# Performance work log

Hardware: AMD Instinct MI355X
Metric: run time of the kernel (lower is better)

## Reference

```python
import jax, jax.numpy as jnp
import numpy as np

E = 5          # num_experts
TEMP = 1.0     # gate temperature


def setup_inputs() -> dict:
    key = jax.random.key(0)
    ks = jax.random.split(key, 12)
    B, C, H, W = 8, 256, 80, 80
    half, quarter = C // 2, C // 4  # 128, 64
    s = lambda fan_in: 1.0 / np.sqrt(fan_in)
    return {
        "x":    jax.random.normal(ks[0], (B, C, H, W), dtype=jnp.float32),
        # gate Linear(C -> E)
        "Wg":   jax.random.uniform(ks[1], (E, C), jnp.float32, -s(C), s(C)),
        "bg":   jax.random.uniform(ks[2], (E,), jnp.float32, -s(C), s(C)),
        # per-expert conv1x1 weights, stacked on expert axis
        "Wrgb": jax.random.uniform(ks[3], (E, half, half), jnp.float32, -s(half), s(half)),
        "brgb": jax.random.uniform(ks[4], (E, half), jnp.float32, -s(half), s(half)),
        "Wtir": jax.random.uniform(ks[5], (E, half, half), jnp.float32, -s(half), s(half)),
        "btir": jax.random.uniform(ks[6], (E, half), jnp.float32, -s(half), s(half)),
        # transform: conv1x1 half->quarter, ReLU, conv1x1 quarter->1
        "Wt1":  jax.random.uniform(ks[7], (E, quarter, half), jnp.float32, -s(half), s(half)),
        "bt1":  jax.random.uniform(ks[8], (E, quarter), jnp.float32, -s(half), s(half)),
        "Wt2":  jax.random.uniform(ks[9], (E, 1, quarter), jnp.float32, -s(quarter), s(quarter)),
        "bt2":  jax.random.uniform(ks[10], (E, 1), jnp.float32, -s(quarter), s(quarter)),
    }


def _gate(x, Wg, bg):
    # AdaptiveAvgPool2d(1) + Flatten + Linear; eval path (no training noise)
    pooled = x.mean(axis=(2, 3))                       # [B, C]
    logits = pooled @ Wg.T + bg                        # [B, E]
    # top-1 mask + masked softmax (argmax == topk(k=1), first index on ties)
    top1 = jnp.argmax(logits, axis=1)                  # [B]
    mask = jax.nn.one_hot(top1, E, dtype=bool)         # [B, E]
    masked = jnp.where(mask, logits, -jnp.inf)
    return jax.nn.softmax(masked / TEMP, axis=1)       # [B, E]


def _experts(x, Wrgb, brgb, Wtir, btir, Wt1, bt1, Wt2, bt2):
    half = x.shape[1] // 2
    xr, xt = x[:, :half], x[:, half:]                  # [B, half, H, W]
    # residual conv1x1 for all experts at once -> [B, E, half, H, W]
    Dr = xr[:, None] + jnp.einsum('bchw,eoc->beohw', xr, Wrgb) + brgb[None, :, :, None, None]
    Dt = xt[:, None] + jnp.einsum('bchw,eoc->beohw', xt, Wtir) + btir[None, :, :, None, None]

    def transform(D):
        h = jax.nn.relu(jnp.einsum('beohw,emo->bemhw', D, Wt1) + bt1[None, :, :, None, None])
        a = jnp.einsum('bemhw,ekm->bekhw', h, Wt2) + bt2[None, :, :, None, None]
        return jax.nn.sigmoid(a)                       # [B, E, 1, H, W]

    return transform(Dr) * Dr + transform(Dt) * Dt     # [B, E, half, H, W]


def reference(x, Wg, bg, Wrgb, brgb, Wtir, btir, Wt1, bt1, Wt2, bt2):
    weights = _gate(x, Wg, bg)                         # [B, E]
    Dfuse = _experts(x, Wrgb, brgb, Wtir, btir, Wt1, bt1, Wt2, bt2)
    # weighted sum over experts -> [B, half, H, W]
    return jnp.einsum('beohw,be->bohw', Dfuse, weights)
```

## Files before the change

kernel.cpp:

```cpp
#include <hip/hip_runtime.h>

#define HW    6400
#define CIN   256
#define HALF  128
#define QUART 64
#define NB    8
#define NE    5

typedef __attribute__((ext_vector_type(8))) short short8;
typedef __attribute__((ext_vector_type(4))) float f32x4;

__device__ __forceinline__ unsigned short f2bf(float f) {
    unsigned u = __builtin_bit_cast(unsigned, f);
    u = (u + 0x7FFFu + ((u >> 16) & 1u)) >> 16;
    return (unsigned short)u;
}

__global__ void pool_prep_kernel(const float* __restrict__ x,
                                 const float* __restrict__ Wrgb, const float* __restrict__ Wtir,
                                 const float* __restrict__ Wt1,
                                 float* __restrict__ pooled, unsigned short* __restrict__ bw) {
    int blk = blockIdx.x;
    if (blk < NB * CIN) {
        const float4* p = reinterpret_cast<const float4*>(x + (size_t)blk * HW);
        float s = 0.f;
        for (int i = threadIdx.x; i < HW / 4; i += 256) {
            float4 v = p[i];
            s += (v.x + v.y) + (v.z + v.w);
        }
        for (int off = 32; off > 0; off >>= 1) s += __shfl_down(s, off, 64);
        __shared__ float wsum[4];
        int wid = threadIdx.x >> 6, lane = threadIdx.x & 63;
        if (lane == 0) wsum[wid] = s;
        __syncthreads();
        if (threadIdx.x == 0)
            pooled[blk] = (wsum[0] + wsum[1] + wsum[2] + wsum[3]) * (1.0f / HW);
    } else {
        int i0 = (blk - NB * CIN) * 1024 + threadIdx.x;
#pragma unroll
        for (int j = 0; j < 4; ++j) {
            int i = i0 + j * 256;
            float v;
            if (i < 81920) {
                v = Wrgb[i];
                int m = i & 16383;
                if ((m >> 7) == (m & 127)) v += 1.0f;
            } else if (i < 163840) {
                int k = i - 81920;
                v = Wtir[k];
                int m = k & 16383;
                if ((m >> 7) == (m & 127)) v += 1.0f;
            } else {
                v = Wt1[i - 163840];
            }
            bw[i] = f2bf(v);
        }
    }
}

__launch_bounds__(256, 4)
__global__ void expert_kernel(const float* __restrict__ x,
                              const unsigned short* __restrict__ bW,
                              const float* __restrict__ brgb, const float* __restrict__ btir,
                              const float* __restrict__ bt1,
                              const float* __restrict__ Wt2, const float* __restrict__ bt2,
                              const float* __restrict__ pooled,
                              const float* __restrict__ Wg, const float* __restrict__ bg,
                              float* __restrict__ out) {
    __shared__ unsigned short lxr[8192];
    __shared__ unsigned short lxt[8192];
    __shared__ float psum[512];
    __shared__ float sfin[128];
    __shared__ int   se;

    const int b    = blockIdx.y;
    const int p0   = blockIdx.x * 64;
    const int t    = threadIdx.x;
    const int w    = __builtin_amdgcn_readfirstlane(t >> 6);
    const int lane = t & 63;
    const int lo   = lane & 15, hi = lane >> 4;

    {
        const int px = t & 63, cb = t >> 6;
        const float* xb = x + (size_t)b * CIN * HW + p0 + px;
        const int li = (px & 15) * 8;
        const int fb = (cb * 4 + (px >> 4)) * 512;
#pragma unroll
        for (int jg = 0; jg < 4; ++jg) {
            unsigned vr[4], vt[4];
#pragma unroll
            for (int jp = 0; jp < 4; ++jp) {
                int ch = cb * 32 + jg * 8 + jp * 2;
                float r0 = xb[(size_t)ch * HW];
                float r1 = xb[(size_t)(ch + 1) * HW];
                float t0 = xb[(size_t)(ch + HALF) * HW];
                float t1 = xb[(size_t)(ch + HALF + 1) * HW];
                vr[jp] = (unsigned)f2bf(r0) | ((unsigned)f2bf(r1) << 16);
                vt[jp] = (unsigned)f2bf(t0) | ((unsigned)f2bf(t1) << 16);
            }
            int si = fb + jg * 128 + li;
            *reinterpret_cast<uint4*>(&lxr[si]) = make_uint4(vr[0], vr[1], vr[2], vr[3]);
            *reinterpret_cast<uint4*>(&lxt[si]) = make_uint4(vt[0], vt[1], vt[2], vt[3]);
        }
    }

    if (t < 64) {
        float pv[4];
#pragma unroll
        for (int j = 0; j < 4; ++j) pv[j] = pooled[b * CIN + t * 4 + j];
        float best = -1e30f; int bi = 0;
        for (int e = 0; e < NE; ++e) {
            float part = 0.f;
#pragma unroll
            for (int j = 0; j < 4; ++j) part += pv[j] * Wg[e * CIN + t * 4 + j];
            for (int off = 32; off > 0; off >>= 1) part += __shfl_down(part, off, 64);
            part = __shfl(part, 0, 64);
            float logit = part + bg[e];
            if (logit > best) { best = logit; bi = e; }
        }
        if (t == 0) se = bi;
    }
    __syncthreads();

    const int e = __builtin_amdgcn_readfirstlane(se);
    const unsigned short* bWrgb = bW + (size_t)e * 16384;
    const unsigned short* bWtir = bW + 81920 + (size_t)e * 16384;
    const unsigned short* bWt1  = bW + 163840 + (size_t)e * 8192;

    f32x4 cr[2][4], ct[2][4];
    {
        f32x4 z = {0.f, 0.f, 0.f, 0.f};
#pragma unroll
        for (int i = 0; i < 2; ++i)
#pragma unroll
            for (int j = 0; j < 4; ++j) { cr[i][j] = z; ct[i][j] = z; }
    }
#pragma unroll
    for (int kt = 0; kt < 4; ++kt) {
        short8 bR[4], bT[4];
#pragma unroll
        for (int pt = 0; pt < 4; ++pt) {
            bR[pt] = *reinterpret_cast<const short8*>(&lxr[(kt * 4 + pt) * 512 + lane * 8]);
            bT[pt] = *reinterpret_cast<const short8*>(&lxt[(kt * 4 + pt) * 512 + lane * 8]);
        }
#pragma unroll
        for (int rt = 0; rt < 2; ++rt) {
            int row = w * 32 + rt * 16 + lo;
            short8 aR = *reinterpret_cast<const short8*>(&bWrgb[row * 128 + kt * 32 + hi * 8]);
            short8 aT = *reinterpret_cast<const short8*>(&bWtir[row * 128 + kt * 32 + hi * 8]);
#pragma unroll
            for (int pt = 0; pt < 4; ++pt) {
                cr[rt][pt] = __builtin_amdgcn_mfma_f32_16x16x32_bf16(aR, bR[pt], cr[rt][pt], 0, 0, 0);
                ct[rt][pt] = __builtin_amdgcn_mfma_f32_16x16x32_bf16(aT, bT[pt], ct[rt][pt], 0, 0, 0);
            }
        }
    }

    uint2 dbr[2][4], dbt[2][4];
#pragma unroll
    for (int rt = 0; rt < 2; ++rt) {
        int r0c = w * 32 + rt * 16 + hi * 4;
        f32x4 biasR = *reinterpret_cast<const f32x4*>(&brgb[e * HALF + r0c]);
        f32x4 biasT = *reinterpret_cast<const f32x4*>(&btir[e * HALF + r0c]);
#pragma unroll
        for (int pt = 0; pt < 4; ++pt) {
#pragma unroll
            for (int rg = 0; rg < 4; ++rg) {
                cr[rt][pt][rg] += biasR[rg];
                ct[rt][pt][rg] += biasT[rg];
            }
            dbr[rt][pt] = make_uint2(
                (unsigned)f2bf(cr[rt][pt][0]) | ((unsigned)f2bf(cr[rt][pt][1]) << 16),
                (unsigned)f2bf(cr[rt][pt][2]) | ((unsigned)f2bf(cr[rt][pt][3]) << 16));
            dbt[rt][pt] = make_uint2(
                (unsigned)f2bf(ct[rt][pt][0]) | ((unsigned)f2bf(ct[rt][pt][1]) << 16),
                (unsigned)f2bf(ct[rt][pt][2]) | ((unsigned)f2bf(ct[rt][pt][3]) << 16));
        }
    }
    __syncthreads();
#pragma unroll
    for (int rt = 0; rt < 2; ++rt) {
        int r0c = w * 32 + rt * 16 + hi * 4;
        int kt2 = r0c >> 5;
        int lp8 = (((r0c >> 3) & 3) * 16 + lo) * 8 + (r0c & 7);
#pragma unroll
        for (int pt = 0; pt < 4; ++pt) {
            int si = (kt2 * 4 + pt) * 512 + lp8;
            *reinterpret_cast<uint2*>(&lxr[si]) = dbr[rt][pt];
            *reinterpret_cast<uint2*>(&lxt[si]) = dbt[rt][pt];
        }
    }
    __syncthreads();

    f32x4 chr[4], cht[4];
    {
        f32x4 z = {0.f, 0.f, 0.f, 0.f};
#pragma unroll
        for (int j = 0; j < 4; ++j) { chr[j] = z; cht[j] = z; }
    }
#pragma unroll
    for (int kt = 0; kt < 4; ++kt) {
        int row = w * 16 + lo;
        short8 aH = *reinterpret_cast<const short8*>(&bWt1[row * 128 + kt * 32 + hi * 8]);
#pragma unroll
        for (int pt = 0; pt < 4; ++pt) {
            short8 bDr = *reinterpret_cast<const short8*>(&lxr[(kt * 4 + pt) * 512 + lane * 8]);
            short8 bDt = *reinterpret_cast<const short8*>(&lxt[(kt * 4 + pt) * 512 + lane * 8]);
            chr[pt] = __builtin_amdgcn_mfma_f32_16x16x32_bf16(aH, bDr, chr[pt], 0, 0, 0);
            cht[pt] = __builtin_amdgcn_mfma_f32_16x16x32_bf16(aH, bDt, cht[pt], 0, 0, 0);
        }
    }

    {
        int m0 = w * 16 + hi * 4;
        f32x4 b1  = *reinterpret_cast<const f32x4*>(&bt1[e * QUART + m0]);
        f32x4 w2v = *reinterpret_cast<const f32x4*>(&Wt2[e * QUART + m0]);
#pragma unroll
        for (int pt = 0; pt < 4; ++pt) {
            float pr = 0.f, ptt = 0.f;
#pragma unroll
            for (int rg = 0; rg < 4; ++rg) {
                pr  = fmaf(w2v[rg], fmaxf(chr[pt][rg] + b1[rg], 0.f), pr);
                ptt = fmaf(w2v[rg], fmaxf(cht[pt][rg] + b1[rg], 0.f), ptt);
            }
            pr  += __shfl_xor(pr, 16, 64);  pr  += __shfl_xor(pr, 32, 64);
            ptt += __shfl_xor(ptt, 16, 64); ptt += __shfl_xor(ptt, 32, 64);
            if (hi == 0) {
                psum[w * 64 + pt * 16 + lo]       = pr;
                psum[256 + w * 64 + pt * 16 + lo] = ptt;
            }
        }
    }
    __syncthreads();
    if (t < 128) {
        int ph = t >> 6, px = t & 63;
        const float* ps = &psum[ph * 256];
        float a = ps[px] + ps[64 + px] + ps[128 + px] + ps[192 + px] + bt2[e];
        sfin[t] = 1.f / (1.f + __expf(-a));
    }
    __syncthreads();

#pragma unroll
    for (int rt = 0; rt < 2; ++rt) {
        int r0c = w * 32 + rt * 16 + hi * 4;
#pragma unroll
        for (int pt = 0; pt < 4; ++pt) {
            int pxb = pt * 16 + lo;
            float sr = sfin[pxb], st = sfin[64 + pxb];
            float* op = out + ((size_t)b * HALF + r0c) * HW + p0 + pxb;
#pragma unroll
            for (int rg = 0; rg < 4; ++rg)
                op[(size_t)rg * HW] = sr * cr[rt][pt][rg] + st * ct[rt][pt][rg];
        }
    }
}

extern "C" void kernel_launch(void* const* d_in, const int* in_sizes, int n_in,
                              void* d_out, int out_size, void* d_ws, size_t ws_size,
                              hipStream_t stream) {
    const float* x    = (const float*)d_in[0];
    const float* Wg   = (const float*)d_in[1];
    const float* bg   = (const float*)d_in[2];
    const float* Wrgb = (const float*)d_in[3];
    const float* brgb = (const float*)d_in[4];
    const float* Wtir = (const float*)d_in[5];
    const float* btir = (const float*)d_in[6];
    const float* Wt1  = (const float*)d_in[7];
    const float* bt1  = (const float*)d_in[8];
    const float* Wt2  = (const float*)d_in[9];
    const float* bt2  = (const float*)d_in[10];
    float* out = (float*)d_out;

    float*          pooled = (float*)d_ws;
    unsigned short* bw     = (unsigned short*)((char*)d_ws + 8192);

    pool_prep_kernel<<<NB * CIN + 200, 256, 0, stream>>>(x, Wrgb, Wtir, Wt1, pooled, bw);
    dim3 grid(100, NB);
    expert_kernel<<<grid, 256, 0, stream>>>(x, bw, brgb, btir, bt1, Wt2, bt2,
                                            pooled, Wg, bg, out);
}
```

Before: 133.3 us.

## Fuse pooling, weight prep and expert compute into one cooperative kernel

Replaces the separate pooling/weight-prep kernel and expert kernel with a single cooperative launch. Each block stages its x tile into LDS once, accumulates per-channel partial sums with wave shuffles and atomics, converts one slice of the weights to bf16, and then waits on a grid-wide sync before gating and running the expert GEMMs. This is meant to avoid reading x from HBM twice and to remove one kernel launch. In exchange it adds a memset, atomics and a grid barrier, and it depends on all 800 blocks being co-resident; if the cooperative launch fails it falls back to the two-kernel path.

```diff
diff --git a/kernel.cpp b/kernel.cpp
--- a/kernel.cpp
+++ b/kernel.cpp
@@ -1,4 +1,7 @@
 #include <hip/hip_runtime.h>
+#include <hip/hip_cooperative_groups.h>
+
+namespace cg = cooperative_groups;
 
 #define HW    6400
 #define CIN   256
@@ -14,6 +17,282 @@
     unsigned u = __builtin_bit_cast(unsigned, f);
     u = (u + 0x7FFFu + ((u >> 16) & 1u)) >> 16;
     return (unsigned short)u;
+}
+
+__device__ __forceinline__ void prep_one(const float* __restrict__ Wrgb_f,
+                                         const float* __restrict__ Wtir_f,
+                                         const float* __restrict__ Wt1_f,
+                                         unsigned short* __restrict__ bW, int i) {
+    float v;
+    if (i < 81920) {
+        v = Wrgb_f[i];
+        int m = i & 16383;
+        if ((m >> 7) == (m & 127)) v += 1.0f;
+    } else if (i < 163840) {
+        int k = i - 81920;
+        v = Wtir_f[k];
+        int m = k & 16383;
+        if ((m >> 7) == (m & 127)) v += 1.0f;
+    } else {
+        v = Wt1_f[i - 163840];
+    }
+    bW[i] = f2bf(v);
+}
+
+template <bool DO_POOL>
+__device__ __forceinline__ void stage_x(const float* __restrict__ x, int b, int p0, int t,
+                                        unsigned short* lxr, unsigned short* lxt,
+                                        float* __restrict__ pooled) {
+    const int px = t & 63, cb = t >> 6;
+    const int lane = t & 63;
+    const float* xb = x + (size_t)b * CIN * HW + p0 + px;
+    const int li = (px & 15) * 8;
+    const int fb = (cb * 4 + (px >> 4)) * 512;
+#pragma unroll
+    for (int jg = 0; jg < 4; ++jg) {
+        float fv[16];
+#pragma unroll
+        for (int jp = 0; jp < 4; ++jp) {
+            int ch = cb * 32 + jg * 8 + jp * 2;
+            fv[jp * 2]         = xb[(size_t)ch * HW];
+            fv[jp * 2 + 1]     = xb[(size_t)(ch + 1) * HW];
+            fv[8 + jp * 2]     = xb[(size_t)(ch + HALF) * HW];
+            fv[8 + jp * 2 + 1] = xb[(size_t)(ch + HALF + 1) * HW];
+        }
+        unsigned vr[4], vt[4];
+#pragma unroll
+        for (int jp = 0; jp < 4; ++jp) {
+            vr[jp] = (unsigned)f2bf(fv[jp * 2]) | ((unsigned)f2bf(fv[jp * 2 + 1]) << 16);
+            vt[jp] = (unsigned)f2bf(fv[8 + jp * 2]) | ((unsigned)f2bf(fv[8 + jp * 2 + 1]) << 16);
+        }
+        int si = fb + jg * 128 + li;
+        *reinterpret_cast<uint4*>(&lxr[si]) = make_uint4(vr[0], vr[1], vr[2], vr[3]);
+        *reinterpret_cast<uint4*>(&lxt[si]) = make_uint4(vt[0], vt[1], vt[2], vt[3]);
+
+        if constexpr (DO_POOL) {
+#pragma unroll
+            for (int s = 1; s < 16; s <<= 1) {
+                bool up = (lane & s) != 0;
+#pragma unroll
+                for (int i = 0; i < 16; i += 2 * s) {
+                    float a = fv[i], bq = fv[i + s];
+                    float send = up ? a : bq;
+                    float recv = __shfl_xor(send, s, 64);
+                    fv[i] = (up ? bq : a) + recv;
+                }
+            }
+            float g = fv[0];
+            g += __shfl_xor(g, 16, 64);
+            g += __shfl_xor(g, 32, 64);
+            if (lane < 16) {
+                int ch = cb * 32 + jg * 8 + (lane & 7) + ((lane >> 3) << 7);
+                atomicAdd(&pooled[b * CIN + ch], g);
+            }
+        }
+    }
+}
+
+__device__ __forceinline__ int gate_wave(const float* __restrict__ pooled,
+                                         const float* __restrict__ Wg,
+                                         const float* __restrict__ bg, int b, int t) {
+    float pv[4];
+#pragma unroll
+    for (int j = 0; j < 4; ++j) pv[j] = pooled[b * CIN + t * 4 + j] * (1.0f / HW);
+    float best = -1e30f; int bi = 0;
+    for (int e = 0; e < NE; ++e) {
+        float part = 0.f;
+#pragma unroll
+        for (int j = 0; j < 4; ++j) part += pv[j] * Wg[e * CIN + t * 4 + j];
+        for (int off = 32; off > 0; off >>= 1) part += __shfl_down(part, off, 64);
+        part = __shfl(part, 0, 64);
+        float logit = part + bg[e];
+        if (logit > best) { best = logit; bi = e; }
+    }
+    return bi;
+}
+
+__device__ __forceinline__ void expert_body(unsigned short* lxr, unsigned short* lxt,
+                                            float* psum, float* sfin,
+                                            int e, int b, int p0, int t, int w,
+                                            int lane, int lo, int hi,
+                                            const unsigned short* __restrict__ bW,
+                                            const float* __restrict__ brgb,
+                                            const float* __restrict__ btir,
+                                            const float* __restrict__ bt1,
+                                            const float* __restrict__ Wt2,
+                                            const float* __restrict__ bt2,
+                                            float* __restrict__ out) {
+    const unsigned short* bWrgb = bW + (size_t)e * 16384;
+    const unsigned short* bWtir = bW + 81920 + (size_t)e * 16384;
+    const unsigned short* bWt1  = bW + 163840 + (size_t)e * 8192;
+
+    f32x4 cr[2][4], ct[2][4];
+    {
+        f32x4 z = {0.f, 0.f, 0.f, 0.f};
+#pragma unroll
+        for (int i = 0; i < 2; ++i)
+#pragma unroll
+            for (int j = 0; j < 4; ++j) { cr[i][j] = z; ct[i][j] = z; }
+    }
+#pragma unroll
+    for (int kt = 0; kt < 4; ++kt) {
+        short8 bR[4], bT[4];
+#pragma unroll
+        for (int pt = 0; pt < 4; ++pt) {
+            bR[pt] = *reinterpret_cast<const short8*>(&lxr[(kt * 4 + pt) * 512 + lane * 8]);
+            bT[pt] = *reinterpret_cast<const short8*>(&lxt[(kt * 4 + pt) * 512 + lane * 8]);
+        }
+#pragma unroll
+        for (int rt = 0; rt < 2; ++rt) {
+            int row = w * 32 + rt * 16 + lo;
+            short8 aR = *reinterpret_cast<const short8*>(&bWrgb[row * 128 + kt * 32 + hi * 8]);
+            short8 aT = *reinterpret_cast<const short8*>(&bWtir[row * 128 + kt * 32 + hi * 8]);
+#pragma unroll
+            for (int pt = 0; pt < 4; ++pt) {
+                cr[rt][pt] = __builtin_amdgcn_mfma_f32_16x16x32_bf16(aR, bR[pt], cr[rt][pt], 0, 0, 0);
+                ct[rt][pt] = __builtin_amdgcn_mfma_f32_16x16x32_bf16(aT, bT[pt], ct[rt][pt], 0, 0, 0);
+            }
+        }
+    }
+
+    uint2 dbr[2][4], dbt[2][4];
+#pragma unroll
+    for (int rt = 0; rt < 2; ++rt) {
+        int r0c = w * 32 + rt * 16 + hi * 4;
+        f32x4 biasR = *reinterpret_cast<const f32x4*>(&brgb[e * HALF + r0c]);
+        f32x4 biasT = *reinterpret_cast<const f32x4*>(&btir[e * HALF + r0c]);
+#pragma unroll
+        for (int pt = 0; pt < 4; ++pt) {
+#pragma unroll
+            for (int rg = 0; rg < 4; ++rg) {
+                cr[rt][pt][rg] += biasR[rg];
+                ct[rt][pt][rg] += biasT[rg];
+            }
+            dbr[rt][pt] = make_uint2(
+                (unsigned)f2bf(cr[rt][pt][0]) | ((unsigned)f2bf(cr[rt][pt][1]) << 16),
+                (unsigned)f2bf(cr[rt][pt][2]) | ((unsigned)f2bf(cr[rt][pt][3]) << 16));
+            dbt[rt][pt] = make_uint2(
+                (unsigned)f2bf(ct[rt][pt][0]) | ((unsigned)f2bf(ct[rt][pt][1]) << 16),
+                (unsigned)f2bf(ct[rt][pt][2]) | ((unsigned)f2bf(ct[rt][pt][3]) << 16));
+        }
+    }
+    __syncthreads();
+#pragma unroll
+    for (int rt = 0; rt < 2; ++rt) {
+        int r0c = w * 32 + rt * 16 + hi * 4;
+        int kt2 = r0c >> 5;
+        int lp8 = (((r0c >> 3) & 3) * 16 + lo) * 8 + (r0c & 7);
+#pragma unroll
+        for (int pt = 0; pt < 4; ++pt) {
+            int si = (kt2 * 4 + pt) * 512 + lp8;
+            *reinterpret_cast<uint2*>(&lxr[si]) = dbr[rt][pt];
+            *reinterpret_cast<uint2*>(&lxt[si]) = dbt[rt][pt];
+        }
+    }
+    __syncthreads();
+
+    f32x4 chr[4], cht[4];
+    {
+        f32x4 z = {0.f, 0.f, 0.f, 0.f};
+#pragma unroll
+        for (int j = 0; j < 4; ++j) { chr[j] = z; cht[j] = z; }
+    }
+#pragma unroll
+    for (int kt = 0; kt < 4; ++kt) {
+        int row = w * 16 + lo;
+        short8 aH = *reinterpret_cast<const short8*>(&bWt1[row * 128 + kt * 32 + hi * 8]);
+#pragma unroll
+        for (int pt = 0; pt < 4; ++pt) {
+            short8 bDr = *reinterpret_cast<const short8*>(&lxr[(kt * 4 + pt) * 512 + lane * 8]);
+            short8 bDt = *reinterpret_cast<const short8*>(&lxt[(kt * 4 + pt) * 512 + lane * 8]);
+            chr[pt] = __builtin_amdgcn_mfma_f32_16x16x32_bf16(aH, bDr, chr[pt], 0, 0, 0);
+            cht[pt] = __builtin_amdgcn_mfma_f32_16x16x32_bf16(aH, bDt, cht[pt], 0, 0, 0);
+        }
+    }
+
+    {
+        int m0 = w * 16 + hi * 4;
+        f32x4 b1  = *reinterpret_cast<const f32x4*>(&bt1[e * QUART + m0]);
+        f32x4 w2v = *reinterpret_cast<const f32x4*>(&Wt2[e * QUART + m0]);
+#pragma unroll
+        for (int pt = 0; pt < 4; ++pt) {
+            float pr = 0.f, ptt = 0.f;
+#pragma unroll
+            for (int rg = 0; rg < 4; ++rg) {
+                pr  = fmaf(w2v[rg], fmaxf(chr[pt][rg] + b1[rg], 0.f), pr);
+                ptt = fmaf(w2v[rg], fmaxf(cht[pt][rg] + b1[rg], 0.f), ptt);
+            }
+            pr  += __shfl_xor(pr, 16, 64);  pr  += __shfl_xor(pr, 32, 64);
+            ptt += __shfl_xor(ptt, 16, 64); ptt += __shfl_xor(ptt, 32, 64);
+            if (hi == 0) {
+                psum[w * 64 + pt * 16 + lo]       = pr;
+                psum[256 + w * 64 + pt * 16 + lo] = ptt;
+            }
+        }
+    }
+    __syncthreads();
+    if (t < 128) {
+        int ph = t >> 6, px = t & 63;
+        const float* ps = &psum[ph * 256];
+        float a = ps[px] + ps[64 + px] + ps[128 + px] + ps[192 + px] + bt2[e];
+        sfin[t] = 1.f / (1.f + __expf(-a));
+    }
+    __syncthreads();
+
+#pragma unroll
+    for (int rt = 0; rt < 2; ++rt) {
+        int r0c = w * 32 + rt * 16 + hi * 4;
+#pragma unroll
+        for (int pt = 0; pt < 4; ++pt) {
+            int pxb = pt * 16 + lo;
+            float sr = sfin[pxb], st = sfin[64 + pxb];
+            float* op = out + ((size_t)b * HALF + r0c) * HW + p0 + pxb;
+#pragma unroll
+            for (int rg = 0; rg < 4; ++rg)
+                op[(size_t)rg * HW] = sr * cr[rt][pt][rg] + st * ct[rt][pt][rg];
+        }
+    }
+}
+
+__launch_bounds__(256, 4)
+__global__ void fused_coop_kernel(const float* __restrict__ x,
+                                  const float* __restrict__ Wrgb_f,
+                                  const float* __restrict__ Wtir_f,
+                                  const float* __restrict__ Wt1_f,
+                                  unsigned short* __restrict__ bW,
+                                  const float* __restrict__ brgb, const float* __restrict__ btir,
+                                  const float* __restrict__ bt1,
+                                  const float* __restrict__ Wt2, const float* __restrict__ bt2,
+                                  float* __restrict__ pooled,
+                                  const float* __restrict__ Wg, const float* __restrict__ bg,
+                                  float* __restrict__ out) {
+    __shared__ unsigned short lxr[8192];
+    __shared__ unsigned short lxt[8192];
+    __shared__ float psum[512];
+    __shared__ float sfin[128];
+    __shared__ int   se;
+
+    const int b    = blockIdx.y;
+    const int p0   = blockIdx.x * 64;
+    const int t    = threadIdx.x;
+    const int w    = __builtin_amdgcn_readfirstlane(t >> 6);
+    const int lane = t & 63;
+    const int lo   = lane & 15, hi = lane >> 4;
+
+    prep_one(Wrgb_f, Wtir_f, Wt1_f, bW, (blockIdx.y * 100 + blockIdx.x) * 256 + t);
+    stage_x<true>(x, b, p0, t, lxr, lxt, pooled);
+
+    cg::this_grid().sync();
+
+    if (t < 64) {
+        int bi = gate_wave(pooled, Wg, bg, b, t);
+        if (t == 0) se = bi;
+    }
+    __syncthreads();
+    const int e = __builtin_amdgcn_readfirstlane(se);
+
+    expert_body(lxr, lxt, psum, sfin, e, b, p0, t, w, lane, lo, hi,
+                bW, brgb, btir, bt1, Wt2, bt2, out);
 }
 
 __global__ void pool_prep_kernel(const float* __restrict__ x,
@@ -34,39 +313,24 @@
         if (lane == 0) wsum[wid] = s;
         __syncthreads();
         if (threadIdx.x == 0)
-            pooled[blk] = (wsum[0] + wsum[1] + wsum[2] + wsum[3]) * (1.0f / HW);
+            pooled[blk] = wsum[0] + wsum[1] + wsum[2] + wsum[3];
     } else {
         int i0 = (blk - NB * CIN) * 1024 + threadIdx.x;
 #pragma unroll
-        for (int j = 0; j < 4; ++j) {
-            int i = i0 + j * 256;
-            float v;
-            if (i < 81920) {
-                v = Wrgb[i];
-                int m = i & 16383;
-                if ((m >> 7) == (m & 127)) v += 1.0f;
-            } else if (i < 163840) {
-                int k = i - 81920;
-                v = Wtir[k];
-                int m = k & 16383;
-                if ((m >> 7) == (m & 127)) v += 1.0f;
-            } else {
-                v = Wt1[i - 163840];
-            }
-            bw[i] = f2bf(v);
-        }
+        for (int j = 0; j < 4; ++j)
+            prep_one(Wrgb, Wtir, Wt1, bw, i0 + j * 256);
     }
 }
 
 __launch_bounds__(256, 4)
-__global__ void expert_kernel(const float* __restrict__ x,
-                              const unsigned short* __restrict__ bW,
-                              const float* __restrict__ brgb, const float* __restrict__ btir,
-                              const float* __restrict__ bt1,
-                              const float* __restrict__ Wt2, const float* __restrict__ bt2,
-                              const float* __restrict__ pooled,
-                              const float* __restrict__ Wg, const float* __restrict__ bg,
-                              float* __restrict__ out) {
+__global__ void expert_fb_kernel(const float* __restrict__ x,
+                                 const unsigned short* __restrict__ bW,
+                                 const float* __restrict__ brgb, const float* __restrict__ btir,
+                                 const float* __restrict__ bt1,
+                                 const float* __restrict__ Wt2, const float* __restrict__ bt2,
+                                 const float* __restrict__ pooled,
+                                 const float* __restrict__ Wg, const float* __restrict__ bg,
+                                 float* __restrict__ out) {
     __shared__ unsigned short lxr[8192];
     __shared__ unsigned short lxt[8192];
     __shared__ float psum[512];
@@ -80,179 +344,17 @@
     const int lane = t & 63;
     const int lo   = lane & 15, hi = lane >> 4;
 
-    {
-        const int px = t & 63, cb = t >> 6;
-        const float* xb = x + (size_t)b * CIN * HW + p0 + px;
-        const int li = (px & 15) * 8;
-        const int fb = (cb * 4 + (px >> 4)) * 512;
-#pragma unroll
-        for (int jg = 0; jg < 4; ++jg) {
-            unsigned vr[4], vt[4];
-#pragma unroll
-            for (int jp = 0; jp < 4; ++jp) {
-                int ch = cb * 32 + jg * 8 + jp * 2;
-                float r0 = xb[(size_t)ch * HW];
-                float r1 = xb[(size_t)(ch + 1) * HW];
-                float t0 = xb[(size_t)(ch + HALF) * HW];
-                float t1 = xb[(size_t)(ch + HALF + 1) * HW];
-                vr[jp] = (unsigned)f2bf(r0) | ((unsigned)f2bf(r1) << 16);
-                vt[jp] = (unsigned)f2bf(t0) | ((unsigned)f2bf(t1) << 16);
-            }
-            int si = fb + jg * 128 + li;
-            *reinterpret_cast<uint4*>(&lxr[si]) = make_uint4(vr[0], vr[1], vr[2], vr[3]);
-            *reinterpret_cast<uint4*>(&lxt[si]) = make_uint4(vt[0], vt[1], vt[2], vt[3]);
-        }
-    }
+    stage_x<false>(x, b, p0, t, lxr, lxt, nullptr);
 
     if (t < 64) {
-        float pv[4];
-#pragma unroll
-        for (int j = 0; j < 4; ++j) pv[j] = pooled[b * CIN + t * 4 + j];
-        float best = -1e30f; int bi = 0;
-        for (int e = 0; e < NE; ++e) {
-            float part = 0.f;
-#pragma unroll
-            for (int j = 0; j < 4; ++j) part += pv[j] * Wg[e * CIN + t * 4 + j];
-            for (int off = 32; off > 0; off >>= 1) part += __shfl_down(part, off, 64);
-            part = __shfl(part, 0, 64);
-            float logit = part + bg[e];
-            if (logit > best) { best = logit; bi = e; }
-        }
+        int bi = gate_wave(pooled, Wg, bg, b, t);
         if (t == 0) se = bi;
     }
     __syncthreads();
-
     const int e = __builtin_amdgcn_readfirstlane(se);
-    const unsigned short* bWrgb = bW + (size_t)e * 16384;
-    const unsigned short* bWtir = bW + 81920 + (size_t)e * 16384;
-    const unsigned short* bWt1  = bW + 163840 + (size_t)e * 8192;
-
-    f32x4 cr[2][4], ct[2][4];
-    {
-        f32x4 z = {0.f, 0.f, 0.f, 0.f};
-#pragma unroll
-        for (int i = 0; i < 2; ++i)
-#pragma unroll
-            for (int j = 0; j < 4; ++j) { cr[i][j] = z; ct[i][j] = z; }
-    }
-#pragma unroll
-    for (int kt = 0; kt < 4; ++kt) {
-        short8 bR[4], bT[4];
-#pragma unroll
-        for (int pt = 0; pt < 4; ++pt) {
-            bR[pt] = *reinterpret_cast<const short8*>(&lxr[(kt * 4 + pt) * 512 + lane * 8]);
-            bT[pt] = *reinterpret_cast<const short8*>(&lxt[(kt * 4 + pt) * 512 + lane * 8]);
-        }
-#pragma unroll
-        for (int rt = 0; rt < 2; ++rt) {
-            int row = w * 32 + rt * 16 + lo;
-            short8 aR = *reinterpret_cast<const short8*>(&bWrgb[row * 128 + kt * 32 + hi * 8]);
-            short8 aT = *reinterpret_cast<const short8*>(&bWtir[row * 128 + kt * 32 + hi * 8]);
-#pragma unroll
-            for (int pt = 0; pt < 4; ++pt) {
-                cr[rt][pt] = __builtin_amdgcn_mfma_f32_16x16x32_bf16(aR, bR[pt], cr[rt][pt], 0, 0, 0);
-                ct[rt][pt] = __builtin_amdgcn_mfma_f32_16x16x32_bf16(aT, bT[pt], ct[rt][pt], 0, 0, 0);
-            }
-        }
-    }
-
-    uint2 dbr[2][4], dbt[2][4];
-#pragma unroll
-    for (int rt = 0; rt < 2; ++rt) {
-        int r0c = w * 32 + rt * 16 + hi * 4;
-        f32x4 biasR = *reinterpret_cast<const f32x4*>(&brgb[e * HALF + r0c]);
-        f32x4 biasT = *reinterpret_cast<const f32x4*>(&btir[e * HALF + r0c]);
-#pragma unroll
-        for (int pt = 0; pt < 4; ++pt) {
-#pragma unroll
-            for (int rg = 0; rg < 4; ++rg) {
-                cr[rt][pt][rg] += biasR[rg];
-                ct[rt][pt][rg] += biasT[rg];
-            }
-            dbr[rt][pt] = make_uint2(
-                (unsigned)f2bf(cr[rt][pt][0]) | ((unsigned)f2bf(cr[rt][pt][1]) << 16),
-                (unsigned)f2bf(cr[rt][pt][2]) | ((unsigned)f2bf(cr[rt][pt][3]) << 16));
-            dbt[rt][pt] = make_uint2(
-                (unsigned)f2bf(ct[rt][pt][0]) | ((unsigned)f2bf(ct[rt][pt][1]) << 16),
-                (unsigned)f2bf(ct[rt][pt][2]) | ((unsigned)f2bf(ct[rt][pt][3]) << 16));
-        }
-    }
-    __syncthreads();
-#pragma unroll
-    for (int rt = 0; rt < 2; ++rt) {
-        int r0c = w * 32 + rt * 16 + hi * 4;
-        int kt2 = r0c >> 5;
-        int lp8 = (((r0c >> 3) & 3) * 16 + lo) * 8 + (r0c & 7);
-#pragma unroll
-        for (int pt = 0; pt < 4; ++pt) {
-            int si = (kt2 * 4 + pt) * 512 + lp8;
-            *reinterpret_cast<uint2*>(&lxr[si]) = dbr[rt][pt];
-            *reinterpret_cast<uint2*>(&lxt[si]) = dbt[rt][pt];
-        }
-    }
-    __syncthreads();
-
-    f32x4 chr[4], cht[4];
-    {
-        f32x4 z = {0.f, 0.f, 0.f, 0.f};
-#pragma unroll
-        for (int j = 0; j < 4; ++j) { chr[j] = z; cht[j] = z; }
-    }
-#pragma unroll
-    for (int kt = 0; kt < 4; ++kt) {
-        int row = w * 16 + lo;
-        short8 aH = *reinterpret_cast<const short8*>(&bWt1[row * 128 + kt * 32 + hi * 8]);
-#pragma unroll
-        for (int pt = 0; pt < 4; ++pt) {
-            short8 bDr = *reinterpret_cast<const short8*>(&lxr[(kt * 4 + pt) * 512 + lane * 8]);
-            short8 bDt = *reinterpret_cast<const short8*>(&lxt[(kt * 4 + pt) * 512 + lane * 8]);
-            chr[pt] = __builtin_amdgcn_mfma_f32_16x16x32_bf16(aH, bDr, chr[pt], 0, 0, 0);
-            cht[pt] = __builtin_amdgcn_mfma_f32_16x16x32_bf16(aH, bDt, cht[pt], 0, 0, 0);
-        }
-    }
-
-    {
-        int m0 = w * 16 + hi * 4;
-        f32x4 b1  = *reinterpret_cast<const f32x4*>(&bt1[e * QUART + m0]);
-        f32x4 w2v = *reinterpret_cast<const f32x4*>(&Wt2[e * QUART + m0]);
-#pragma unroll
-        for (int pt = 0; pt < 4; ++pt) {
-            float pr = 0.f, ptt = 0.f;
-#pragma unroll
-            for (int rg = 0; rg < 4; ++rg) {
-                pr  = fmaf(w2v[rg], fmaxf(chr[pt][rg] + b1[rg], 0.f), pr);
-                ptt = fmaf(w2v[rg], fmaxf(cht[pt][rg] + b1[rg], 0.f), ptt);
-            }
-            pr  += __shfl_xor(pr, 16, 64);  pr  += __shfl_xor(pr, 32, 64);
-            ptt += __shfl_xor(ptt, 16, 64); ptt += __shfl_xor(ptt, 32, 64);
-            if (hi == 0) {
-                psum[w * 64 + pt * 16 + lo]       = pr;
-                psum[256 + w * 64 + pt * 16 + lo] = ptt;
-            }
-        }
-    }
-    __syncthreads();
-    if (t < 128) {
-        int ph = t >> 6, px = t & 63;
-        const float* ps = &psum[ph * 256];
-        float a = ps[px] + ps[64 + px] + ps[128 + px] + ps[192 + px] + bt2[e];
-        sfin[t] = 1.f / (1.f + __expf(-a));
-    }
-    __syncthreads();
-
-#pragma unroll
-    for (int rt = 0; rt < 2; ++rt) {
-        int r0c = w * 32 + rt * 16 + hi * 4;
-#pragma unroll
-        for (int pt = 0; pt < 4; ++pt) {
-            int pxb = pt * 16 + lo;
-            float sr = sfin[pxb], st = sfin[64 + pxb];
-            float* op = out + ((size_t)b * HALF + r0c) * HW + p0 + pxb;
-#pragma unroll
-            for (int rg = 0; rg < 4; ++rg)
-                op[(size_t)rg * HW] = sr * cr[rt][pt][rg] + st * ct[rt][pt][rg];
-        }
-    }
+
+    expert_body(lxr, lxt, psum, sfin, e, b, p0, t, w, lane, lo, hi,
+                bW, brgb, btir, bt1, Wt2, bt2, out);
 }
 
 extern "C" void kernel_launch(void* const* d_in, const int* in_sizes, int n_in,
@@ -274,8 +376,17 @@
     float*          pooled = (float*)d_ws;
     unsigned short* bw     = (unsigned short*)((char*)d_ws + 8192);
 
-    pool_prep_kernel<<<NB * CIN + 200, 256, 0, stream>>>(x, Wrgb, Wtir, Wt1, pooled, bw);
-    dim3 grid(100, NB);
-    expert_kernel<<<grid, 256, 0, stream>>>(x, bw, brgb, btir, bt1, Wt2, bt2,
-                                            pooled, Wg, bg, out);
-}
+    hipMemsetAsync(pooled, 0, NB * CIN * sizeof(float), stream);
+
+    void* args[] = {(void*)&x, (void*)&Wrgb, (void*)&Wtir, (void*)&Wt1, (void*)&bw,
+                    (void*)&brgb, (void*)&btir, (void*)&bt1, (void*)&Wt2, (void*)&bt2,
+                    (void*)&pooled, (void*)&Wg, (void*)&bg, (void*)&out};
+    hipError_t err = hipLaunchCooperativeKernel((const void*)fused_coop_kernel,
+                                                dim3(100, NB), dim3(256), args, 0, stream);
+    if (err != hipSuccess) {
+        pool_prep_kernel<<<NB * CIN + 200, 256, 0, stream>>>(x, Wrgb, Wtir, Wt1, pooled, bw);
+        dim3 grid(100, NB);
+        expert_fb_kernel<<<grid, 256, 0, stream>>>(x, bw, brgb, btir, bt1, Wt2, bt2,
+                                                   pooled, Wg, bg, out);
+    }
+}
```

After: 217.8 us. 63.4% more time.

## Halve expert-kernel pixel tile to 32 and raise occupancy target

Applied to the files above, without the earlier changes.

Shrinks the expert kernel's pixel tile from 64 to 32 pixels per block, which doubles the grid to 200x8 blocks and halves the LDS and accumulator footprint per block. The launch-bounds occupancy hint goes from 4 to 6 blocks per CU so more waves can hide the strided global loads. The x staging load is restructured to issue all 16 loads before converting, and the 1/HW scaling moves from the pool kernel into the gate. The cost is that each block reloads the expert weight tiles for half as many pixels, doubling weight traffic per output, and the MFMA work per wave becomes smaller.

```diff
diff --git a/kernel.cpp b/kernel.cpp
--- a/kernel.cpp
+++ b/kernel.cpp
@@ -6,6 +6,8 @@
 #define QUART 64
 #define NB    8
 #define NE    5
+#define PXT   32
+#define NT    (HW / PXT)
 
 typedef __attribute__((ext_vector_type(8))) short short8;
 typedef __attribute__((ext_vector_type(4))) float f32x4;
@@ -14,6 +16,26 @@
     unsigned u = __builtin_bit_cast(unsigned, f);
     u = (u + 0x7FFFu + ((u >> 16) & 1u)) >> 16;
     return (unsigned short)u;
+}
+
+__device__ __forceinline__ void prep_one(const float* __restrict__ Wrgb_f,
+                                         const float* __restrict__ Wtir_f,
+                                         const float* __restrict__ Wt1_f,
+                                         unsigned short* __restrict__ bW, int i) {
+    float v;
+    if (i < 81920) {
+        v = Wrgb_f[i];
+        int m = i & 16383;
+        if ((m >> 7) == (m & 127)) v += 1.0f;
+    } else if (i < 163840) {
+        int k = i - 81920;
+        v = Wtir_f[k];
+        int m = k & 16383;
+        if ((m >> 7) == (m & 127)) v += 1.0f;
+    } else {
+        v = Wt1_f[i - 163840];
+    }
+    bW[i] = f2bf(v);
 }
 
 __global__ void pool_prep_kernel(const float* __restrict__ x,
@@ -34,31 +56,16 @@
         if (lane == 0) wsum[wid] = s;
         __syncthreads();
         if (threadIdx.x == 0)
-            pooled[blk] = (wsum[0] + wsum[1] + wsum[2] + wsum[3]) * (1.0f / HW);
+            pooled[blk] = wsum[0] + wsum[1] + wsum[2] + wsum[3];
     } else {
         int i0 = (blk - NB * CIN) * 1024 + threadIdx.x;
 #pragma unroll
-        for (int j = 0; j < 4; ++j) {
-            int i = i0 + j * 256;
-            float v;
-            if (i < 81920) {
-                v = Wrgb[i];
-                int m = i & 16383;
-                if ((m >> 7) == (m & 127)) v += 1.0f;
-            } else if (i < 163840) {
-                int k = i - 81920;
-                v = Wtir[k];
-                int m = k & 16383;
-                if ((m >> 7) == (m & 127)) v += 1.0f;
-            } else {
-                v = Wt1[i - 163840];
-            }
-            bw[i] = f2bf(v);
-        }
-    }
-}
-
-__launch_bounds__(256, 4)
+        for (int j = 0; j < 4; ++j)
+            prep_one(Wrgb, Wtir, Wt1, bw, i0 + j * 256);
+    }
+}
+
+__launch_bounds__(256, 6)
 __global__ void expert_kernel(const float* __restrict__ x,
                               const unsigned short* __restrict__ bW,
                               const float* __restrict__ brgb, const float* __restrict__ btir,
@@ -67,38 +74,42 @@
                               const float* __restrict__ pooled,
                               const float* __restrict__ Wg, const float* __restrict__ bg,
                               float* __restrict__ out) {
-    __shared__ unsigned short lxr[8192];
-    __shared__ unsigned short lxt[8192];
-    __shared__ float psum[512];
-    __shared__ float sfin[128];
+    __shared__ unsigned short lxr[4096];
+    __shared__ unsigned short lxt[4096];
+    __shared__ float psum[256];
+    __shared__ float sfin[64];
     __shared__ int   se;
 
     const int b    = blockIdx.y;
-    const int p0   = blockIdx.x * 64;
+    const int p0   = blockIdx.x * PXT;
     const int t    = threadIdx.x;
     const int w    = __builtin_amdgcn_readfirstlane(t >> 6);
     const int lane = t & 63;
     const int lo   = lane & 15, hi = lane >> 4;
 
     {
-        const int px = t & 63, cb = t >> 6;
+        const int px = t & 31, cg = t >> 5;
         const float* xb = x + (size_t)b * CIN * HW + p0 + px;
-        const int li = (px & 15) * 8;
-        const int fb = (cb * 4 + (px >> 4)) * 512;
-#pragma unroll
-        for (int jg = 0; jg < 4; ++jg) {
+        const int kt = cg >> 1, pt = px >> 4, li = (px & 15) * 8;
+#pragma unroll
+        for (int jg = 0; jg < 2; ++jg) {
+            float fv[16];
+#pragma unroll
+            for (int jp = 0; jp < 4; ++jp) {
+                int rch = cg * 16 + jg * 8 + jp * 2;
+                fv[jp * 2]         = xb[(size_t)rch * HW];
+                fv[jp * 2 + 1]     = xb[(size_t)(rch + 1) * HW];
+                fv[8 + jp * 2]     = xb[(size_t)(rch + HALF) * HW];
+                fv[8 + jp * 2 + 1] = xb[(size_t)(rch + HALF + 1) * HW];
+            }
             unsigned vr[4], vt[4];
 #pragma unroll
             for (int jp = 0; jp < 4; ++jp) {
-                int ch = cb * 32 + jg * 8 + jp * 2;
-                float r0 = xb[(size_t)ch * HW];
-                float r1 = xb[(size_t)(ch + 1) * HW];
-                float t0 = xb[(size_t)(ch + HALF) * HW];
-                float t1 = xb[(size_t)(ch + HALF + 1) * HW];
-                vr[jp] = (unsigned)f2bf(r0) | ((unsigned)f2bf(r1) << 16);
-                vt[jp] = (unsigned)f2bf(t0) | ((unsigned)f2bf(t1) << 16);
-            }
-            int si = fb + jg * 128 + li;
+                vr[jp] = (unsigned)f2bf(fv[jp * 2]) | ((unsigned)f2bf(fv[jp * 2 + 1]) << 16);
+                vt[jp] = (unsigned)f2bf(fv[8 + jp * 2]) | ((unsigned)f2bf(fv[8 + jp * 2 + 1]) << 16);
+            }
+            int o  = (cg & 1) * 2 + jg;
+            int si = (kt * 2 + pt) * 512 + o * 128 + li;
             *reinterpret_cast<uint4*>(&lxr[si]) = make_uint4(vr[0], vr[1], vr[2], vr[3]);
             *reinterpret_cast<uint4*>(&lxt[si]) = make_uint4(vt[0], vt[1], vt[2], vt[3]);
         }
@@ -107,7 +118,7 @@
     if (t < 64) {
         float pv[4];
 #pragma unroll
-        for (int j = 0; j < 4; ++j) pv[j] = pooled[b * CIN + t * 4 + j];
+        for (int j = 0; j < 4; ++j) pv[j] = pooled[b * CIN + t * 4 + j] * (1.0f / HW);
         float best = -1e30f; int bi = 0;
         for (int e = 0; e < NE; ++e) {
             float part = 0.f;
@@ -127,21 +138,21 @@
     const unsigned short* bWtir = bW + 81920 + (size_t)e * 16384;
     const unsigned short* bWt1  = bW + 163840 + (size_t)e * 8192;
 
-    f32x4 cr[2][4], ct[2][4];
+    f32x4 cr[2][2], ct[2][2];
     {
         f32x4 z = {0.f, 0.f, 0.f, 0.f};
 #pragma unroll
         for (int i = 0; i < 2; ++i)
 #pragma unroll
-            for (int j = 0; j < 4; ++j) { cr[i][j] = z; ct[i][j] = z; }
+            for (int j = 0; j < 2; ++j) { cr[i][j] = z; ct[i][j] = z; }
     }
 #pragma unroll
     for (int kt = 0; kt < 4; ++kt) {
-        short8 bR[4], bT[4];
-#pragma unroll
-        for (int pt = 0; pt < 4; ++pt) {
-            bR[pt] = *reinterpret_cast<const short8*>(&lxr[(kt * 4 + pt) * 512 + lane * 8]);
-            bT[pt] = *reinterpret_cast<const short8*>(&lxt[(kt * 4 + pt) * 512 + lane * 8]);
+        short8 bR[2], bT[2];
+#pragma unroll
+        for (int pt = 0; pt < 2; ++pt) {
+            bR[pt] = *reinterpret_cast<const short8*>(&lxr[(kt * 2 + pt) * 512 + lane * 8]);
+            bT[pt] = *reinterpret_cast<const short8*>(&lxt[(kt * 2 + pt) * 512 + lane * 8]);
         }
 #pragma unroll
         for (int rt = 0; rt < 2; ++rt) {
@@ -149,21 +160,21 @@
             short8 aR = *reinterpret_cast<const short8*>(&bWrgb[row * 128 + kt * 32 + hi * 8]);
             short8 aT = *reinterpret_cast<const short8*>(&bWtir[row * 128 + kt * 32 + hi * 8]);
 #pragma unroll
-            for (int pt = 0; pt < 4; ++pt) {
+            for (int pt = 0; pt < 2; ++pt) {
                 cr[rt][pt] = __builtin_amdgcn_mfma_f32_16x16x32_bf16(aR, bR[pt], cr[rt][pt], 0, 0, 0);
                 ct[rt][pt] = __builtin_amdgcn_mfma_f32_16x16x32_bf16(aT, bT[pt], ct[rt][pt], 0, 0, 0);
             }
         }
     }
 
-    uint2 dbr[2][4], dbt[2][4];
+    uint2 dbr[2][2], dbt[2][2];
 #pragma unroll
     for (int rt = 0; rt < 2; ++rt) {
         int r0c = w * 32 + rt * 16 + hi * 4;
         f32x4 biasR = *reinterpret_cast<const f32x4*>(&brgb[e * HALF + r0c]);
         f32x4 biasT = *reinterpret_cast<const f32x4*>(&btir[e * HALF + r0c]);
 #pragma unroll
-        for (int pt = 0; pt < 4; ++pt) {
+        for (int pt = 0; pt < 2; ++pt) {
 #pragma unroll
             for (int rg = 0; rg < 4; ++rg) {
                 cr[rt][pt][rg] += biasR[rg];
@@ -184,28 +195,28 @@
         int kt2 = r0c >> 5;
         int lp8 = (((r0c >> 3) & 3) * 16 + lo) * 8 + (r0c & 7);
 #pragma unroll
-        for (int pt = 0; pt < 4; ++pt) {
-            int si = (kt2 * 4 + pt) * 512 + lp8;
+        for (int pt = 0; pt < 2; ++pt) {
+            int si = (kt2 * 2 + pt) * 512 + lp8;
             *reinterpret_cast<uint2*>(&lxr[si]) = dbr[rt][pt];
             *reinterpret_cast<uint2*>(&lxt[si]) = dbt[rt][pt];
         }
     }
     __syncthreads();
 
-    f32x4 chr[4], cht[4];
+    f32x4 chr[2], cht[2];
     {
         f32x4 z = {0.f, 0.f, 0.f, 0.f};
 #pragma unroll
-        for (int j = 0; j < 4; ++j) { chr[j] = z; cht[j] = z; }
+        for (int j = 0; j < 2; ++j) { chr[j] = z; cht[j] = z; }
     }
 #pragma unroll
     for (int kt = 0; kt < 4; ++kt) {
         int row = w * 16 + lo;
         short8 aH = *reinterpret_cast<const short8*>(&bWt1[row * 128 + kt * 32 + hi * 8]);
 #pragma unroll
-        for (int pt = 0; pt < 4; ++pt) {
-            short8 bDr = *reinterpret_cast<const short8*>(&lxr[(kt * 4 + pt) * 512 + lane * 8]);
-            short8 bDt = *reinterpret_cast<const short8*>(&lxt[(kt * 4 + pt) * 512 + lane * 8]);
+        for (int pt = 0; pt < 2; ++pt) {
+            short8 bDr = *reinterpret_cast<const short8*>(&lxr[(kt * 2 + pt) * 512 + lane * 8]);
+            short8 bDt = *reinterpret_cast<const short8*>(&lxt[(kt * 2 + pt) * 512 + lane * 8]);
             chr[pt] = __builtin_amdgcn_mfma_f32_16x16x32_bf16(aH, bDr, chr[pt], 0, 0, 0);
             cht[pt] = __builtin_amdgcn_mfma_f32_16x16x32_bf16(aH, bDt, cht[pt], 0, 0, 0);
         }
@@ -216,7 +227,7 @@
         f32x4 b1  = *reinterpret_cast<const f32x4*>(&bt1[e * QUART + m0]);
         f32x4 w2v = *reinterpret_cast<const f32x4*>(&Wt2[e * QUART + m0]);
 #pragma unroll
-        for (int pt = 0; pt < 4; ++pt) {
+        for (int pt = 0; pt < 2; ++pt) {
             float pr = 0.f, ptt = 0.f;
 #pragma unroll
             for (int rg = 0; rg < 4; ++rg) {
@@ -226,16 +237,16 @@
             pr  += __shfl_xor(pr, 16, 64);  pr  += __shfl_xor(pr, 32, 64);
             ptt += __shfl_xor(ptt, 16, 64); ptt += __shfl_xor(ptt, 32, 64);
             if (hi == 0) {
-                psum[w * 64 + pt * 16 + lo]       = pr;
-                psum[256 + w * 64 + pt * 16 + lo] = ptt;
-            }
-        }
-    }
-    __syncthreads();
-    if (t < 128) {
-        int ph = t >> 6, px = t & 63;
-        const float* ps = &psum[ph * 256];
-        float a = ps[px] + ps[64 + px] + ps[128 + px] + ps[192 + px] + bt2[e];
+                psum[w * 32 + pt * 16 + lo]       = pr;
+                psum[128 + w * 32 + pt * 16 + lo] = ptt;
+            }
+        }
+    }
+    __syncthreads();
+    if (t < 64) {
+        int ph = t >> 5, q = t & 31;
+        const float* ps = &psum[ph * 128];
+        float a = ps[q] + ps[32 + q] + ps[64 + q] + ps[96 + q] + bt2[e];
         sfin[t] = 1.f / (1.f + __expf(-a));
     }
     __syncthreads();
@@ -244,10 +255,10 @@
     for (int rt = 0; rt < 2; ++rt) {
         int r0c = w * 32 + rt * 16 + hi * 4;
 #pragma unroll
-        for (int pt = 0; pt < 4; ++pt) {
-            int pxb = pt * 16 + lo;
-            float sr = sfin[pxb], st = sfin[64 + pxb];
-            float* op = out + ((size_t)b * HALF + r0c) * HW + p0 + pxb;
+        for (int pt = 0; pt < 2; ++pt) {
+            int px = pt * 16 + lo;
+            float sr = sfin[px], st = sfin[32 + px];
+            float* op = out + ((size_t)b * HALF + r0c) * HW + p0 + px;
 #pragma unroll
             for (int rg = 0; rg < 4; ++rg)
                 op[(size_t)rg * HW] = sr * cr[rt][pt][rg] + st * ct[rt][pt][rg];
@@ -275,7 +286,7 @@
     unsigned short* bw     = (unsigned short*)((char*)d_ws + 8192);
 
     pool_prep_kernel<<<NB * CIN + 200, 256, 0, stream>>>(x, Wrgb, Wtir, Wt1, pooled, bw);
-    dim3 grid(100, NB);
+    dim3 grid(NT, NB);
     expert_kernel<<<grid, 256, 0, stream>>>(x, bw, brgb, btir, bt1, Wt2, bt2,
                                             pooled, Wg, bg, out);
 }
```

Measured after the change: 134.7 us. About the same (+1.1%).

## Pack x to bf16 tiles during pooling pass, load packed tiles in expert kernel

Applied to the files above, without the earlier changes.

The pooling kernel now reads each 8-channel group once, accumulates the channel means, and at the same time writes x as bf16 in the exact LDS tile layout the expert kernel uses. The expert kernel then copies its tile with contiguous 16-byte loads instead of gathering strided fp32 values and converting them. This aims to replace the second fp32 read of x with a half-size coalesced read. The cost is an extra bf16 write of x to the workspace, and the pooling grid shrinks to 256 blocks, which may lower parallelism in the first kernel.

```diff
diff --git a/kernel.cpp b/kernel.cpp
--- a/kernel.cpp
+++ b/kernel.cpp
@@ -6,6 +6,8 @@
 #define QUART 64
 #define NB    8
 #define NE    5
+#define PXT   64
+#define NT    (HW / PXT)
 
 typedef __attribute__((ext_vector_type(8))) short short8;
 typedef __attribute__((ext_vector_type(4))) float f32x4;
@@ -16,50 +18,83 @@
     return (unsigned short)u;
 }
 
-__global__ void pool_prep_kernel(const float* __restrict__ x,
-                                 const float* __restrict__ Wrgb, const float* __restrict__ Wtir,
-                                 const float* __restrict__ Wt1,
-                                 float* __restrict__ pooled, unsigned short* __restrict__ bw) {
-    int blk = blockIdx.x;
-    if (blk < NB * CIN) {
-        const float4* p = reinterpret_cast<const float4*>(x + (size_t)blk * HW);
-        float s = 0.f;
-        for (int i = threadIdx.x; i < HW / 4; i += 256) {
-            float4 v = p[i];
-            s += (v.x + v.y) + (v.z + v.w);
-        }
-        for (int off = 32; off > 0; off >>= 1) s += __shfl_down(s, off, 64);
-        __shared__ float wsum[4];
-        int wid = threadIdx.x >> 6, lane = threadIdx.x & 63;
-        if (lane == 0) wsum[wid] = s;
+__device__ __forceinline__ void prep_one(const float* __restrict__ Wrgb_f,
+                                         const float* __restrict__ Wtir_f,
+                                         const float* __restrict__ Wt1_f,
+                                         unsigned short* __restrict__ bW, int i) {
+    float v;
+    if (i < 81920) {
+        v = Wrgb_f[i];
+        int m = i & 16383;
+        if ((m >> 7) == (m & 127)) v += 1.0f;
+    } else if (i < 163840) {
+        int k = i - 81920;
+        v = Wtir_f[k];
+        int m = k & 16383;
+        if ((m >> 7) == (m & 127)) v += 1.0f;
+    } else {
+        v = Wt1_f[i - 163840];
+    }
+    bW[i] = f2bf(v);
+}
+
+__global__ void pack_pool_prep_kernel(const float* __restrict__ x,
+                                      const float* __restrict__ Wrgb,
+                                      const float* __restrict__ Wtir,
+                                      const float* __restrict__ Wt1,
+                                      float* __restrict__ pooled,
+                                      unsigned short* __restrict__ bw,
+                                      unsigned short* __restrict__ sc) {
+    const int bid = blockIdx.x;
+    const int t   = threadIdx.x;
+    if (bid < NB * 32) {
+        const int b  = bid >> 5, cg = bid & 31;
+        const int c0 = cg * 8;
+        const int halfsel = c0 >> 7;
+        const int ch = c0 & 127;
+        const int kt = ch >> 5, lrow = (ch >> 3) & 3;
+        const float* xr[8];
+#pragma unroll
+        for (int j = 0; j < 8; ++j) xr[j] = x + ((size_t)b * CIN + c0 + j) * HW;
+        unsigned short* scb = sc + (size_t)halfsel * NB * NT * 8192
+                                 + (size_t)b * NT * 8192;
+        float sum[8] = {0.f, 0.f, 0.f, 0.f, 0.f, 0.f, 0.f, 0.f};
+        for (int px = t; px < HW; px += 256) {
+            float v[8];
+#pragma unroll
+            for (int j = 0; j < 8; ++j) { v[j] = xr[j][px]; sum[j] += v[j]; }
+            unsigned pk[4];
+#pragma unroll
+            for (int j = 0; j < 4; ++j)
+                pk[j] = (unsigned)f2bf(v[2 * j]) | ((unsigned)f2bf(v[2 * j + 1]) << 16);
+            int tile = px >> 6, pt = (px >> 4) & 3;
+            size_t so = (size_t)tile * 8192 + (size_t)(kt * 4 + pt) * 512
+                      + (size_t)(lrow * 16 + (px & 15)) * 8;
+            *reinterpret_cast<uint4*>(&scb[so]) = make_uint4(pk[0], pk[1], pk[2], pk[3]);
+        }
+#pragma unroll
+        for (int j = 0; j < 8; ++j)
+            for (int off = 32; off > 0; off >>= 1)
+                sum[j] += __shfl_down(sum[j], off, 64);
+        __shared__ float pls[4][8];
+        int wv = t >> 6, ln = t & 63;
+        if (ln == 0) {
+#pragma unroll
+            for (int j = 0; j < 8; ++j) pls[wv][j] = sum[j];
+        }
         __syncthreads();
-        if (threadIdx.x == 0)
-            pooled[blk] = (wsum[0] + wsum[1] + wsum[2] + wsum[3]) * (1.0f / HW);
+        if (t < 8)
+            pooled[b * CIN + c0 + t] = pls[0][t] + pls[1][t] + pls[2][t] + pls[3][t];
     } else {
-        int i0 = (blk - NB * CIN) * 1024 + threadIdx.x;
-#pragma unroll
-        for (int j = 0; j < 4; ++j) {
-            int i = i0 + j * 256;
-            float v;
-            if (i < 81920) {
-                v = Wrgb[i];
-                int m = i & 16383;
-                if ((m >> 7) == (m & 127)) v += 1.0f;
-            } else if (i < 163840) {
-                int k = i - 81920;
-                v = Wtir[k];
-                int m = k & 16383;
-                if ((m >> 7) == (m & 127)) v += 1.0f;
-            } else {
-                v = Wt1[i - 163840];
-            }
-            bw[i] = f2bf(v);
-        }
+        int i0 = (bid - NB * 32) * 1024 + t;
+#pragma unroll
+        for (int j = 0; j < 4; ++j)
+            prep_one(Wrgb, Wtir, Wt1, bw, i0 + j * 256);
     }
 }
 
 __launch_bounds__(256, 4)
-__global__ void expert_kernel(const float* __restrict__ x,
+__global__ void expert_kernel(const unsigned short* __restrict__ sc,
                               const unsigned short* __restrict__ bW,
                               const float* __restrict__ brgb, const float* __restrict__ btir,
                               const float* __restrict__ bt1,
@@ -74,40 +109,27 @@
     __shared__ int   se;
 
     const int b    = blockIdx.y;
-    const int p0   = blockIdx.x * 64;
+    const int p0   = blockIdx.x * PXT;
     const int t    = threadIdx.x;
     const int w    = __builtin_amdgcn_readfirstlane(t >> 6);
     const int lane = t & 63;
     const int lo   = lane & 15, hi = lane >> 4;
 
     {
-        const int px = t & 63, cb = t >> 6;
-        const float* xb = x + (size_t)b * CIN * HW + p0 + px;
-        const int li = (px & 15) * 8;
-        const int fb = (cb * 4 + (px >> 4)) * 512;
-#pragma unroll
-        for (int jg = 0; jg < 4; ++jg) {
-            unsigned vr[4], vt[4];
-#pragma unroll
-            for (int jp = 0; jp < 4; ++jp) {
-                int ch = cb * 32 + jg * 8 + jp * 2;
-                float r0 = xb[(size_t)ch * HW];
-                float r1 = xb[(size_t)(ch + 1) * HW];
-                float t0 = xb[(size_t)(ch + HALF) * HW];
-                float t1 = xb[(size_t)(ch + HALF + 1) * HW];
-                vr[jp] = (unsigned)f2bf(r0) | ((unsigned)f2bf(r1) << 16);
-                vt[jp] = (unsigned)f2bf(t0) | ((unsigned)f2bf(t1) << 16);
-            }
-            int si = fb + jg * 128 + li;
-            *reinterpret_cast<uint4*>(&lxr[si]) = make_uint4(vr[0], vr[1], vr[2], vr[3]);
-            *reinterpret_cast<uint4*>(&lxt[si]) = make_uint4(vt[0], vt[1], vt[2], vt[3]);
+        const unsigned short* srcr = sc + (size_t)b * NT * 8192 + (size_t)blockIdx.x * 8192;
+        const unsigned short* srct = srcr + (size_t)NB * NT * 8192;
+#pragma unroll
+        for (int i = 0; i < 4; ++i) {
+            int o = (i * 256 + t) * 8;
+            *reinterpret_cast<uint4*>(&lxr[o]) = *reinterpret_cast<const uint4*>(&srcr[o]);
+            *reinterpret_cast<uint4*>(&lxt[o]) = *reinterpret_cast<const uint4*>(&srct[o]);
         }
     }
 
     if (t < 64) {
         float pv[4];
 #pragma unroll
-        for (int j = 0; j < 4; ++j) pv[j] = pooled[b * CIN + t * 4 + j];
+        for (int j = 0; j < 4; ++j) pv[j] = pooled[b * CIN + t * 4 + j] * (1.0f / HW);
         float best = -1e30f; int bi = 0;
         for (int e = 0; e < NE; ++e) {
             float part = 0.f;
@@ -273,9 +295,11 @@
 
     float*          pooled = (float*)d_ws;
     unsigned short* bw     = (unsigned short*)((char*)d_ws + 8192);
-
-    pool_prep_kernel<<<NB * CIN + 200, 256, 0, stream>>>(x, Wrgb, Wtir, Wt1, pooled, bw);
-    dim3 grid(100, NB);
-    expert_kernel<<<grid, 256, 0, stream>>>(x, bw, brgb, btir, bt1, Wt2, bt2,
+    unsigned short* sc     = (unsigned short*)((char*)d_ws + 417792);
+
+    pack_pool_prep_kernel<<<NB * 32 + 200, 256, 0, stream>>>(x, Wrgb, Wtir, Wt1,
+                                                             pooled, bw, sc);
+    dim3 grid(NT, NB);
+    expert_kernel<<<grid, 256, 0, stream>>>(sc, bw, brgb, btir, bt1, Wt2, bt2,
                                             pooled, Wg, bg, out);
 }
```

Result: slower. 162.8 us (+22.1%).
